# Optimization experiments

Hardware: AMD Instinct MI355X
Metric: run time of the kernel (lower is better)

Reference implementation:

```python
import jax, jax.numpy as jnp
import numpy as np


def setup_inputs() -> dict:
    key = jax.random.key(0)
    ks = jax.random.split(key, 4)
    B, C, H, W = 8, 256, 64, 64
    Cq = C // 8
    x = jax.random.normal(ks[0], (B, C, H, W), dtype=jnp.float32)
    wq = jax.random.normal(ks[1], (Cq, C), dtype=jnp.float32) * (1.0 / np.sqrt(C))
    bq = jnp.zeros((Cq,), dtype=jnp.float32)
    wk = jax.random.normal(ks[2], (Cq, C), dtype=jnp.float32) * (1.0 / np.sqrt(C))
    bk = jnp.zeros((Cq,), dtype=jnp.float32)
    wv = jax.random.normal(ks[3], (C, C), dtype=jnp.float32) * (1.0 / np.sqrt(C))
    bv = jnp.zeros((C,), dtype=jnp.float32)
    return {"x": x, "wq": wq, "bq": bq, "wk": wk, "bk": bk, "wv": wv, "bv": bv}


def reference(x, wq, bq, wk, bk, wv, bv):
    B, C, H, W = x.shape
    N = H * W
    xf = x.reshape(B, C, N)  # [B, C, N] ; 1x1 conv == channel matmul
    q = jnp.einsum('bcn,dc->bnd', xf, wq) + bq          # [B, N, Cq]
    k = jnp.einsum('bcn,dc->bdn', xf, wk) + bk[:, None]  # [B, Cq, N]
    v = jnp.einsum('bcn,dc->bdn', xf, wv) + bv[:, None]  # [B, C, N]
    energy = jnp.einsum('bnd,bdm->bnm', q, k)           # [B, N, N]
    attn = jax.nn.softmax(energy, axis=-1)              # softmax over keys
    # out[b,c,i] = sum_j v[b,c,j] * attn[b,i,j]
    out = jnp.einsum('bcj,bij->bci', v, attn).reshape(B, C, H, W)
    return x + out
```

## Files before the change

kernel.cpp:

```cpp
#include <hip/hip_runtime.h>


#define CH  256
#define DQ  32
#define NSP 4096
#define RWS 320

typedef short short8 __attribute__((ext_vector_type(8)));
typedef float float4v __attribute__((ext_vector_type(4)));

__device__ __forceinline__ unsigned short f2b(float f) {
  unsigned int u = __float_as_uint(f);
  unsigned int r = u + 0x7fffu + ((u >> 16) & 1u);
  return (unsigned short)(r >> 16);
}
__device__ __forceinline__ short8 ld8(const unsigned short* p) {
  return *(const short8*)p;
}

__global__ __launch_bounds__(256) void prep_kernel(
    const float* __restrict__ wq, const float* __restrict__ bq,
    const float* __restrict__ wk, const float* __restrict__ bk,
    const float* __restrict__ wv, const float* __restrict__ bv,
    unsigned short* __restrict__ wh, unsigned short* __restrict__ wl,
    float* __restrict__ ball) {
  int r = blockIdx.x, c = threadIdx.x;
  float v;
  if (r < 32)       v = wq[r * CH + c];
  else if (r < 64)  v = wk[(r - 32) * CH + c];
  else              v = wv[(r - 64) * CH + c];
  unsigned int u = __float_as_uint(v);
  unsigned short hi = (unsigned short)(u >> 16);
  float hf = __uint_as_float(u & 0xffff0000u);
  unsigned short lo = (unsigned short)(__float_as_uint(v - hf) >> 16);
  wh[r * CH + c] = hi;
  wl[r * CH + c] = lo;
  if (c == 0)
    ball[r] = (r < 32) ? bq[r] : (r < 64 ? bk[r - 32] : bv[r - 64]);
}

__device__ __forceinline__ void stage_x32(const float* xkn, float* buf,
                                          int w, int lane) {
  const int c = 8 * w + (lane >> 3);
  const int n = (4 * (lane & 7)) ^ ((w & 3) << 3);
  const float* gp = xkn + (size_t)c * NSP + n;
  __builtin_amdgcn_global_load_lds(
      (const __attribute__((address_space(1))) unsigned int*)gp,
      (__attribute__((address_space(3))) unsigned int*)(buf + w * 256),
      16, 0, 0);
}

__global__ __launch_bounds__(256, 3) void proj_kernel(
    const float* __restrict__ x,
    const unsigned short* __restrict__ wh, const unsigned short* __restrict__ wl,
    const float* __restrict__ ball,
    unsigned short* __restrict__ qb, unsigned short* __restrict__ kb,
    unsigned short* __restrict__ vb, int b0) {
  __shared__ float xs[2][1024];

  const int bz   = blockIdx.z;
  const int bg   = b0 + bz;
  const int n0   = blockIdx.x * 32;
  const int t    = threadIdx.x;
  const int w    = t >> 6;
  const int lane = t & 63;
  const int col  = lane & 15;
  const int quad = lane >> 4;
  const int r0   = 80 * w;
  const int rb0  = quad * 256 + (col ^ (8 * (quad & 1)));
  const int nsx  = quad >> 1;

  const float* xb = x + (size_t)bg * CH * NSP;

  float4v acc[5][2];
#pragma unroll
  for (int rf = 0; rf < 5; ++rf) {
    float bias = ball[r0 + 16 * rf + col];
#pragma unroll
    for (int ns = 0; ns < 2; ++ns)
      acc[rf][ns] = (float4v){bias, bias, bias, bias};
  }

  stage_x32(xb + n0, xs[0], w, lane);
  __syncthreads();
  int cur = 0;

#pragma unroll 1
  for (int ks = 0; ks < 8; ++ks) {
    const int k0 = ks * 32;
    if (ks < 7)
      stage_x32(xb + (size_t)(k0 + 32) * NSP + n0, xs[cur ^ 1], w, lane);

    short8 wfh[5], wfl[5];
#pragma unroll
    for (int rf = 0; rf < 5; ++rf) {
      size_t wo = (size_t)(r0 + 16 * rf + col) * CH + k0 + quad * 8;
      wfh[rf] = ld8(wh + wo);
      wfl[rf] = ld8(wl + wo);
    }

    const float* xc = &xs[cur][0];
    short8 ah[2], al[2];
#pragma unroll
    for (int nsb = 0; nsb < 2; ++nsb) {
      const float* xp2 = xc + rb0 + 16 * (nsb ^ nsx);
#pragma unroll
      for (int j = 0; j < 8; ++j) {
        float v = xp2[j * 32];
        unsigned int u = __float_as_uint(v);
        ah[nsb][j] = (short)(u >> 16);
        float hf = __uint_as_float(u & 0xffff0000u);
        al[nsb][j] = (short)(__float_as_uint(v - hf) >> 16);
      }
    }

#pragma unroll
    for (int rf = 0; rf < 5; ++rf)
#pragma unroll
      for (int ns = 0; ns < 2; ++ns) {
        acc[rf][ns] = __builtin_amdgcn_mfma_f32_16x16x32_bf16(ah[ns], wfh[rf], acc[rf][ns], 0, 0, 0);
        acc[rf][ns] = __builtin_amdgcn_mfma_f32_16x16x32_bf16(al[ns], wfh[rf], acc[rf][ns], 0, 0, 0);
        acc[rf][ns] = __builtin_amdgcn_mfma_f32_16x16x32_bf16(ah[ns], wfl[rf], acc[rf][ns], 0, 0, 0);
      }

    __syncthreads();
    cur ^= 1;
  }

#pragma unroll
  for (int rf = 0; rf < 5; ++rf) {
    const int rr = r0 + 16 * rf + col;
    const int rb = r0 + 16 * rf;
#pragma unroll
    for (int ns = 0; ns < 2; ++ns) {
      const int nb = n0 + ns * 16 + quad * 4;
      if (rb < 32) {
#pragma unroll
        for (int reg = 0; reg < 4; ++reg)
          qb[((size_t)bz * NSP + nb + reg) * DQ + rr] = f2b(acc[rf][ns][reg]);
      } else if (rb < 64) {
#pragma unroll
        for (int reg = 0; reg < 4; ++reg)
          kb[((size_t)bz * NSP + nb + reg) * DQ + (rr - 32)] = f2b(acc[rf][ns][reg]);
      } else {
        ushort4 o = {f2b(acc[rf][ns][0]), f2b(acc[rf][ns][1]),
                     f2b(acc[rf][ns][2]), f2b(acc[rf][ns][3])};
        *(ushort4*)&vb[((size_t)bz * CH + (rr - 64)) * NSP + nb] = o;
      }
    }
  }
}

__global__ __launch_bounds__(512, 4) void attn_kernel(
    const float* __restrict__ x,
    const unsigned short* __restrict__ qb, const unsigned short* __restrict__ kb,
    const unsigned short* __restrict__ vb,
    float* __restrict__ out, int b0, int ns) {
  __shared__ unsigned short ps[2 * 64 * 64];
  __shared__ float buf[4][64];
  __shared__ float lf[64];

  const int bl   = blockIdx.x % ns;
  const int bg   = b0 + bl;
  const int i0   = (blockIdx.x / ns) * 64;
  const int t    = threadIdx.x;
  const int w    = t >> 6;
  const int rh   = w >> 2;
  const int kq   = w & 3;
  const int lane = t & 63;
  const int col  = lane & 15;
  const int quad = lane >> 4;
  const float LOG2E = 1.4426950408889634f;
  const float MOFF  = 57.70780163555852f;

  const unsigned short* qbb = qb + (size_t)bl * NSP * DQ;
  const unsigned short* kbb = kb + (size_t)bl * NSP * DQ;
  const unsigned short* vbb = vb + (size_t)bl * CH * NSP;

  short8 qf[2];
#pragma unroll
  for (int rgp = 0; rgp < 2; ++rgp)
    qf[rgp] = ld8(qbb + (size_t)(i0 + 32 * rh + 16 * rgp + col) * DQ + quad * 8);
  const float4v z4 = (float4v){0.f, 0.f, 0.f, 0.f};

  const int kb8 = 2 * kq + (col >> 3);
  const int ci  = col & 7;
  const int q4  = 4 * (quad & 1);
  const int ob  = quad ^ ci;

  float4v acc[4][2];
#pragma unroll
  for (int rg = 0; rg < 4; ++rg)
#pragma unroll
    for (int ct = 0; ct < 2; ++ct) acc[rg][ct] = z4;
  float lp[2][4];
#pragma unroll
  for (int rgp = 0; rgp < 2; ++rgp)
#pragma unroll
    for (int reg = 0; reg < 4; ++reg) lp[rgp][reg] = 0.0f;

  short8 kf = ld8(kbb + (size_t)(16 * kq + col) * DQ + quad * 8);
  for (int j0 = 0; j0 < NSP; j0 += 64) {
    const int cp = (j0 >> 6) & 1;
    short8 vf[2][2];
#pragma unroll
    for (int ct = 0; ct < 2; ++ct)
#pragma unroll
      for (int h = 0; h < 2; ++h)
        vf[ct][h] = ld8(vbb + (size_t)(32 * w + 16 * ct + col) * NSP
                        + j0 + 32 * h + quad * 8);
    float4v c0 = __builtin_amdgcn_mfma_f32_16x16x32_bf16(qf[0], kf, z4, 0, 0, 0);
    float4v c1 = __builtin_amdgcn_mfma_f32_16x16x32_bf16(qf[1], kf, z4, 0, 0, 0);
    int jn = (j0 + 64 < NSP) ? j0 + 64 : 0;
    short8 kfn = ld8(kbb + (size_t)(jn + 16 * kq + col) * DQ + quad * 8);
    unsigned short* pw = &ps[cp * 4096 + (32 * rh + quad * 4) * 64 + ci];
#pragma unroll
    for (int reg = 0; reg < 4; ++reg) {
      float p0 = __builtin_amdgcn_exp2f(fmaf(c0[reg], LOG2E, -MOFF));
      float p1 = __builtin_amdgcn_exp2f(fmaf(c1[reg], LOG2E, -MOFF));
      lp[0][reg] += p0;
      lp[1][reg] += p1;
      const int so = reg * 64 + (kb8 ^ (q4 + reg)) * 8;
      pw[so]        = f2b(p0);
      pw[so + 1024] = f2b(p1);
    }
    __syncthreads();

    const short8* pb0 = (const short8*)&ps[cp * 4096 + col * 64 + ob * 8];
    const short8* pb1 = (const short8*)&ps[cp * 4096 + col * 64 + (ob ^ 4) * 8];
    __builtin_amdgcn_s_setprio(1);
#pragma unroll
    for (int rg = 0; rg < 4; ++rg) {
      short8 pf0 = pb0[rg * 128];
      short8 pf1 = pb1[rg * 128];
#pragma unroll
      for (int ct = 0; ct < 2; ++ct) {
        acc[rg][ct] = __builtin_amdgcn_mfma_f32_16x16x32_bf16(pf0, vf[ct][0], acc[rg][ct], 0, 0, 0);
        acc[rg][ct] = __builtin_amdgcn_mfma_f32_16x16x32_bf16(pf1, vf[ct][1], acc[rg][ct], 0, 0, 0);
      }
    }
    __builtin_amdgcn_s_setprio(0);
    kf = kfn;
  }

#pragma unroll
  for (int rgp = 0; rgp < 2; ++rgp)
#pragma unroll
    for (int reg = 0; reg < 4; ++reg) {
#pragma unroll
      for (int mask = 1; mask <= 8; mask <<= 1)
        lp[rgp][reg] += __shfl_xor(lp[rgp][reg], mask);
    }
  if (col == 0) {
#pragma unroll
    for (int rgp = 0; rgp < 2; ++rgp)
#pragma unroll
      for (int reg = 0; reg < 4; ++reg)
        buf[kq][32 * rh + 16 * rgp + quad * 4 + reg] = lp[rgp][reg];
  }
  __syncthreads();
  if (kq == 0 && col == 0) {
#pragma unroll
    for (int rgp = 0; rgp < 2; ++rgp)
#pragma unroll
      for (int reg = 0; reg < 4; ++reg) {
        int row = 32 * rh + 16 * rgp + quad * 4 + reg;
        lf[row] = 1.0f / (buf[0][row] + buf[1][row] + buf[2][row] + buf[3][row]);
      }
  }
  __syncthreads();

#pragma unroll
  for (int rg = 0; rg < 4; ++rg) {
    float linv[4];
#pragma unroll
    for (int reg = 0; reg < 4; ++reg)
      linv[reg] = lf[16 * rg + quad * 4 + reg];
#pragma unroll
    for (int ct = 0; ct < 2; ++ct) {
      int c  = 32 * w + 16 * ct + col;
      int ib = i0 + 16 * rg + quad * 4;
      size_t idx = ((size_t)bg * CH + c) * NSP + ib;
      float4 xr = *(const float4*)&x[idx];
      float4 o;
      o.x = acc[rg][ct][0] * linv[0] + xr.x;
      o.y = acc[rg][ct][1] * linv[1] + xr.y;
      o.z = acc[rg][ct][2] * linv[2] + xr.z;
      o.w = acc[rg][ct][3] * linv[3] + xr.w;
      *(float4*)&out[idx] = o;
    }
  }
}

extern "C" void kernel_launch(void* const* d_in, const int* in_sizes, int n_in,
                              void* d_out, int out_size, void* d_ws, size_t ws_size,
                              hipStream_t stream) {
  (void)in_sizes; (void)n_in; (void)out_size;
  const float* x  = (const float*)d_in[0];
  const float* wq = (const float*)d_in[1];
  const float* bq = (const float*)d_in[2];
  const float* wk = (const float*)d_in[3];
  const float* bk = (const float*)d_in[4];
  const float* wv = (const float*)d_in[5];
  const float* bv = (const float*)d_in[6];
  float* out = (float*)d_out;

  const size_t WALL_B = (size_t)RWS * CH * sizeof(float) + 4096;
  const size_t QB_B = (size_t)NSP * DQ * sizeof(unsigned short);
  const size_t VB_B = (size_t)CH * NSP * sizeof(unsigned short);
  const size_t PER_B = 2 * QB_B + VB_B;

  int ns = 8;
  while (ns > 1 && WALL_B + (size_t)ns * PER_B > ws_size) ns >>= 1;

  char* ws = (char*)d_ws;
  unsigned short* wh = (unsigned short*)ws;
  unsigned short* wl = wh + (size_t)RWS * CH;
  float* ball = (float*)(ws + (size_t)RWS * CH * 2 * sizeof(unsigned short));
  char* qkv = ws + WALL_B;
  unsigned short* qb = (unsigned short*)qkv;
  unsigned short* kb = (unsigned short*)(qkv + (size_t)ns * QB_B);
  unsigned short* vb = (unsigned short*)(qkv + (size_t)ns * 2 * QB_B);

  prep_kernel<<<dim3(RWS), dim3(256), 0, stream>>>(wq, bq, wk, bk, wv, bv, wh, wl, ball);
  for (int b0 = 0; b0 < 8; b0 += ns) {
    proj_kernel<<<dim3(128, 1, ns), dim3(256), 0, stream>>>(
        x, wh, wl, ball, qb, kb, vb, b0);
    attn_kernel<<<dim3(64 * ns), dim3(512), 0, stream>>>(
        x, qb, kb, vb, out, b0, ns);
  }
}
```

Baseline: 269.6 us.

## Widen projection tile with full-K LDS staging; shrink attention block to 32 rows

The projection kernel now processes 64 spatial positions per block and stages all eight 32-channel slices of x into LDS up front (64 KB), removing the per-step double-buffer syncs and doubling reuse of weight fragments. The attention kernel moves from 512-thread blocks covering 64 query rows to 256-thread blocks covering 32 rows, each wave owning 64 output channels and all 64 keys per tile, giving twice as many blocks. The trade-offs are lower proj occupancy from the large LDS footprint, more V loads per query row, and recomputation of QK energies across more blocks.

```diff
diff --git a/kernel.cpp b/kernel.cpp
--- a/kernel.cpp
+++ b/kernel.cpp
@@ -39,57 +39,62 @@
     ball[r] = (r < 32) ? bq[r] : (r < 64 ? bk[r - 32] : bv[r - 64]);
 }
 
-__device__ __forceinline__ void stage_x32(const float* xkn, float* buf,
-                                          int w, int lane) {
-  const int c = 8 * w + (lane >> 3);
-  const int n = (4 * (lane & 7)) ^ ((w & 3) << 3);
-  const float* gp = xkn + (size_t)c * NSP + n;
-  __builtin_amdgcn_global_load_lds(
-      (const __attribute__((address_space(1))) unsigned int*)gp,
-      (__attribute__((address_space(3))) unsigned int*)(buf + w * 256),
-      16, 0, 0);
-}
-
-__global__ __launch_bounds__(256, 3) void proj_kernel(
+__device__ __forceinline__ void stage_x(const float* xkn, float* buf,
+                                        int w, int lane) {
+#pragma unroll
+  for (int i = 0; i < 2; ++i) {
+    const int h  = 2 * w + i;
+    const int sw = ((h >> 1) & 1) * 16;
+    const int c  = h * 4 + (lane >> 4);
+    const int n  = ((lane & 15) * 4) ^ sw;
+    const float* gp = xkn + (size_t)c * NSP + n;
+    __builtin_amdgcn_global_load_lds(
+        (const __attribute__((address_space(1))) unsigned int*)gp,
+        (__attribute__((address_space(3))) unsigned int*)(buf + h * 256),
+        16, 0, 0);
+  }
+}
+
+__global__ __launch_bounds__(256, 2) void proj_kernel(
     const float* __restrict__ x,
     const unsigned short* __restrict__ wh, const unsigned short* __restrict__ wl,
     const float* __restrict__ ball,
     unsigned short* __restrict__ qb, unsigned short* __restrict__ kb,
     unsigned short* __restrict__ vb, int b0) {
-  __shared__ float xs[2][1024];
+  __shared__ float xs[8][2048];
 
   const int bz   = blockIdx.z;
   const int bg   = b0 + bz;
-  const int n0   = blockIdx.x * 32;
+  const int n0   = blockIdx.x * 64;
   const int t    = threadIdx.x;
   const int w    = t >> 6;
   const int lane = t & 63;
   const int col  = lane & 15;
   const int quad = lane >> 4;
   const int r0   = 80 * w;
-  const int rb0  = quad * 256 + (col ^ (8 * (quad & 1)));
-  const int nsx  = quad >> 1;
+  const int e    = (quad & 1) * 16;
+  const int lbase = quad * 512 + col;
 
   const float* xb = x + (size_t)bg * CH * NSP;
 
-  float4v acc[5][2];
+#pragma unroll
+  for (int ks = 0; ks < 8; ++ks)
+    stage_x(xb + (size_t)(ks * 32) * NSP + n0, xs[ks], w, lane);
+
+  float4v acc[5][4];
 #pragma unroll
   for (int rf = 0; rf < 5; ++rf) {
     float bias = ball[r0 + 16 * rf + col];
 #pragma unroll
-    for (int ns = 0; ns < 2; ++ns)
+    for (int ns = 0; ns < 4; ++ns)
       acc[rf][ns] = (float4v){bias, bias, bias, bias};
   }
 
-  stage_x32(xb + n0, xs[0], w, lane);
   __syncthreads();
-  int cur = 0;
-
-#pragma unroll 1
+
+#pragma unroll
   for (int ks = 0; ks < 8; ++ks) {
     const int k0 = ks * 32;
-    if (ks < 7)
-      stage_x32(xb + (size_t)(k0 + 32) * NSP + n0, xs[cur ^ 1], w, lane);
 
     short8 wfh[5], wfl[5];
 #pragma unroll
@@ -99,14 +104,14 @@
       wfl[rf] = ld8(wl + wo);
     }
 
-    const float* xc = &xs[cur][0];
-    short8 ah[2], al[2];
-#pragma unroll
-    for (int nsb = 0; nsb < 2; ++nsb) {
-      const float* xp2 = xc + rb0 + 16 * (nsb ^ nsx);
+    const float* xc = &xs[ks][0];
+    short8 ah[4], al[4];
+#pragma unroll
+    for (int nsb = 0; nsb < 4; ++nsb) {
+      const float* xp2 = xc + lbase + ((nsb * 16) ^ e);
 #pragma unroll
       for (int j = 0; j < 8; ++j) {
-        float v = xp2[j * 32];
+        float v = xp2[j * 64];
         unsigned int u = __float_as_uint(v);
         ah[nsb][j] = (short)(u >> 16);
         float hf = __uint_as_float(u & 0xffff0000u);
@@ -117,14 +122,11 @@
 #pragma unroll
     for (int rf = 0; rf < 5; ++rf)
 #pragma unroll
-      for (int ns = 0; ns < 2; ++ns) {
+      for (int ns = 0; ns < 4; ++ns) {
         acc[rf][ns] = __builtin_amdgcn_mfma_f32_16x16x32_bf16(ah[ns], wfh[rf], acc[rf][ns], 0, 0, 0);
         acc[rf][ns] = __builtin_amdgcn_mfma_f32_16x16x32_bf16(al[ns], wfh[rf], acc[rf][ns], 0, 0, 0);
         acc[rf][ns] = __builtin_amdgcn_mfma_f32_16x16x32_bf16(ah[ns], wfl[rf], acc[rf][ns], 0, 0, 0);
       }
-
-    __syncthreads();
-    cur ^= 1;
   }
 
 #pragma unroll
@@ -132,7 +134,7 @@
     const int rr = r0 + 16 * rf + col;
     const int rb = r0 + 16 * rf;
 #pragma unroll
-    for (int ns = 0; ns < 2; ++ns) {
+    for (int ns = 0; ns < 4; ++ns) {
       const int nb = n0 + ns * 16 + quad * 4;
       if (rb < 32) {
 #pragma unroll
@@ -151,22 +153,20 @@
   }
 }
 
-__global__ __launch_bounds__(512, 4) void attn_kernel(
+__global__ __launch_bounds__(256, 4) void attn_kernel(
     const float* __restrict__ x,
     const unsigned short* __restrict__ qb, const unsigned short* __restrict__ kb,
     const unsigned short* __restrict__ vb,
     float* __restrict__ out, int b0, int ns) {
-  __shared__ unsigned short ps[2 * 64 * 64];
-  __shared__ float buf[4][64];
-  __shared__ float lf[64];
+  __shared__ unsigned short ps[2 * 32 * 64];
+  __shared__ float buf[4][32];
+  __shared__ float lf[32];
 
   const int bl   = blockIdx.x % ns;
   const int bg   = b0 + bl;
-  const int i0   = (blockIdx.x / ns) * 64;
+  const int i0   = (blockIdx.x / ns) * 32;
   const int t    = threadIdx.x;
   const int w    = t >> 6;
-  const int rh   = w >> 2;
-  const int kq   = w & 3;
   const int lane = t & 63;
   const int col  = lane & 15;
   const int quad = lane >> 4;
@@ -180,40 +180,40 @@
   short8 qf[2];
 #pragma unroll
   for (int rgp = 0; rgp < 2; ++rgp)
-    qf[rgp] = ld8(qbb + (size_t)(i0 + 32 * rh + 16 * rgp + col) * DQ + quad * 8);
+    qf[rgp] = ld8(qbb + (size_t)(i0 + 16 * rgp + col) * DQ + quad * 8);
   const float4v z4 = (float4v){0.f, 0.f, 0.f, 0.f};
 
-  const int kb8 = 2 * kq + (col >> 3);
+  const int kb8 = 2 * w + (col >> 3);
   const int ci  = col & 7;
   const int q4  = 4 * (quad & 1);
   const int ob  = quad ^ ci;
 
-  float4v acc[4][2];
-#pragma unroll
-  for (int rg = 0; rg < 4; ++rg)
-#pragma unroll
-    for (int ct = 0; ct < 2; ++ct) acc[rg][ct] = z4;
+  float4v acc[2][4];
+#pragma unroll
+  for (int rg = 0; rg < 2; ++rg)
+#pragma unroll
+    for (int ct = 0; ct < 4; ++ct) acc[rg][ct] = z4;
   float lp[2][4];
 #pragma unroll
   for (int rgp = 0; rgp < 2; ++rgp)
 #pragma unroll
     for (int reg = 0; reg < 4; ++reg) lp[rgp][reg] = 0.0f;
 
-  short8 kf = ld8(kbb + (size_t)(16 * kq + col) * DQ + quad * 8);
+  short8 kf = ld8(kbb + (size_t)(16 * w + col) * DQ + quad * 8);
   for (int j0 = 0; j0 < NSP; j0 += 64) {
     const int cp = (j0 >> 6) & 1;
-    short8 vf[2][2];
-#pragma unroll
-    for (int ct = 0; ct < 2; ++ct)
+    short8 vf[4][2];
+#pragma unroll
+    for (int ct = 0; ct < 4; ++ct)
 #pragma unroll
       for (int h = 0; h < 2; ++h)
-        vf[ct][h] = ld8(vbb + (size_t)(32 * w + 16 * ct + col) * NSP
+        vf[ct][h] = ld8(vbb + (size_t)(64 * w + 16 * ct + col) * NSP
                         + j0 + 32 * h + quad * 8);
     float4v c0 = __builtin_amdgcn_mfma_f32_16x16x32_bf16(qf[0], kf, z4, 0, 0, 0);
     float4v c1 = __builtin_amdgcn_mfma_f32_16x16x32_bf16(qf[1], kf, z4, 0, 0, 0);
     int jn = (j0 + 64 < NSP) ? j0 + 64 : 0;
-    short8 kfn = ld8(kbb + (size_t)(jn + 16 * kq + col) * DQ + quad * 8);
-    unsigned short* pw = &ps[cp * 4096 + (32 * rh + quad * 4) * 64 + ci];
+    short8 kfn = ld8(kbb + (size_t)(jn + 16 * w + col) * DQ + quad * 8);
+    unsigned short* pw = &ps[cp * 2048 + (quad * 4) * 64 + ci];
 #pragma unroll
     for (int reg = 0; reg < 4; ++reg) {
       float p0 = __builtin_amdgcn_exp2f(fmaf(c0[reg], LOG2E, -MOFF));
@@ -226,15 +226,15 @@
     }
     __syncthreads();
 
-    const short8* pb0 = (const short8*)&ps[cp * 4096 + col * 64 + ob * 8];
-    const short8* pb1 = (const short8*)&ps[cp * 4096 + col * 64 + (ob ^ 4) * 8];
+    const short8* pb0 = (const short8*)&ps[cp * 2048 + col * 64 + ob * 8];
+    const short8* pb1 = (const short8*)&ps[cp * 2048 + col * 64 + (ob ^ 4) * 8];
     __builtin_amdgcn_s_setprio(1);
 #pragma unroll
-    for (int rg = 0; rg < 4; ++rg) {
+    for (int rg = 0; rg < 2; ++rg) {
       short8 pf0 = pb0[rg * 128];
       short8 pf1 = pb1[rg * 128];
 #pragma unroll
-      for (int ct = 0; ct < 2; ++ct) {
+      for (int ct = 0; ct < 4; ++ct) {
         acc[rg][ct] = __builtin_amdgcn_mfma_f32_16x16x32_bf16(pf0, vf[ct][0], acc[rg][ct], 0, 0, 0);
         acc[rg][ct] = __builtin_amdgcn_mfma_f32_16x16x32_bf16(pf1, vf[ct][1], acc[rg][ct], 0, 0, 0);
       }
@@ -256,29 +256,29 @@
     for (int rgp = 0; rgp < 2; ++rgp)
 #pragma unroll
       for (int reg = 0; reg < 4; ++reg)
-        buf[kq][32 * rh + 16 * rgp + quad * 4 + reg] = lp[rgp][reg];
+        buf[w][16 * rgp + quad * 4 + reg] = lp[rgp][reg];
   }
   __syncthreads();
-  if (kq == 0 && col == 0) {
+  if (w == 0 && col == 0) {
 #pragma unroll
     for (int rgp = 0; rgp < 2; ++rgp)
 #pragma unroll
       for (int reg = 0; reg < 4; ++reg) {
-        int row = 32 * rh + 16 * rgp + quad * 4 + reg;
+        int row = 16 * rgp + quad * 4 + reg;
         lf[row] = 1.0f / (buf[0][row] + buf[1][row] + buf[2][row] + buf[3][row]);
       }
   }
   __syncthreads();
 
 #pragma unroll
-  for (int rg = 0; rg < 4; ++rg) {
+  for (int rg = 0; rg < 2; ++rg) {
     float linv[4];
 #pragma unroll
     for (int reg = 0; reg < 4; ++reg)
       linv[reg] = lf[16 * rg + quad * 4 + reg];
 #pragma unroll
-    for (int ct = 0; ct < 2; ++ct) {
-      int c  = 32 * w + 16 * ct + col;
+    for (int ct = 0; ct < 4; ++ct) {
+      int c  = 64 * w + 16 * ct + col;
       int ib = i0 + 16 * rg + quad * 4;
       size_t idx = ((size_t)bg * CH + c) * NSP + ib;
       float4 xr = *(const float4*)&x[idx];
@@ -324,9 +324,9 @@
 
   prep_kernel<<<dim3(RWS), dim3(256), 0, stream>>>(wq, bq, wk, bk, wv, bv, wh, wl, ball);
   for (int b0 = 0; b0 < 8; b0 += ns) {
-    proj_kernel<<<dim3(128, 1, ns), dim3(256), 0, stream>>>(
+    proj_kernel<<<dim3(64, 1, ns), dim3(256), 0, stream>>>(
         x, wh, wl, ball, qb, kb, vb, b0);
-    attn_kernel<<<dim3(64 * ns), dim3(512), 0, stream>>>(
+    attn_kernel<<<dim3(128 * ns), dim3(256), 0, stream>>>(
         x, qb, kb, vb, out, b0, ns);
   }
 }
```

Measured after the change: 361.5 us. 34.1% more time.

## Stage full x tile up front and transpose Q/K stores through LDS

Applied to the files above, without the earlier changes.

The projection kernel now issues all eight x K-slices into a 32KB LDS buffer at once, replacing the double-buffered loop, so the loop has a single barrier rather than one per step. Weight fragments are loaded in groups of two to cut register pressure, and the occupancy hint rises from 3 to 4 blocks. Q/K results are transposed through LDS so they can be written as vectorized ushort4 rows instead of scattered 2-byte stores. The cost is more LDS per block, which may limit occupancy, and the XOR bank swizzle on x staging is removed, which may bring back LDS bank conflicts.

```diff
diff --git a/kernel.cpp b/kernel.cpp
--- a/kernel.cpp
+++ b/kernel.cpp
@@ -42,7 +42,7 @@
 __device__ __forceinline__ void stage_x32(const float* xkn, float* buf,
                                           int w, int lane) {
   const int c = 8 * w + (lane >> 3);
-  const int n = (4 * (lane & 7)) ^ ((w & 3) << 3);
+  const int n = (lane & 7) * 4;
   const float* gp = xkn + (size_t)c * NSP + n;
   __builtin_amdgcn_global_load_lds(
       (const __attribute__((address_space(1))) unsigned int*)gp,
@@ -50,13 +50,13 @@
       16, 0, 0);
 }
 
-__global__ __launch_bounds__(256, 3) void proj_kernel(
+__global__ __launch_bounds__(256, 4) void proj_kernel(
     const float* __restrict__ x,
     const unsigned short* __restrict__ wh, const unsigned short* __restrict__ wl,
     const float* __restrict__ ball,
     unsigned short* __restrict__ qb, unsigned short* __restrict__ kb,
     unsigned short* __restrict__ vb, int b0) {
-  __shared__ float xs[2][1024];
+  __shared__ float xs[8][1024];
 
   const int bz   = blockIdx.z;
   const int bg   = b0 + bz;
@@ -67,86 +67,106 @@
   const int col  = lane & 15;
   const int quad = lane >> 4;
   const int r0   = 80 * w;
-  const int rb0  = quad * 256 + (col ^ (8 * (quad & 1)));
-  const int nsx  = quad >> 1;
 
   const float* xb = x + (size_t)bg * CH * NSP;
+
+#pragma unroll
+  for (int ks = 0; ks < 8; ++ks)
+    stage_x32(xb + (size_t)(ks * 32) * NSP + n0, xs[ks], w, lane);
 
   float4v acc[5][2];
 #pragma unroll
   for (int rf = 0; rf < 5; ++rf) {
     float bias = ball[r0 + 16 * rf + col];
 #pragma unroll
-    for (int ns = 0; ns < 2; ++ns)
-      acc[rf][ns] = (float4v){bias, bias, bias, bias};
-  }
-
-  stage_x32(xb + n0, xs[0], w, lane);
+    for (int g = 0; g < 2; ++g)
+      acc[rf][g] = (float4v){bias, bias, bias, bias};
+  }
+
   __syncthreads();
-  int cur = 0;
 
 #pragma unroll 1
   for (int ks = 0; ks < 8; ++ks) {
     const int k0 = ks * 32;
-    if (ks < 7)
-      stage_x32(xb + (size_t)(k0 + 32) * NSP + n0, xs[cur ^ 1], w, lane);
-
-    short8 wfh[5], wfl[5];
-#pragma unroll
-    for (int rf = 0; rf < 5; ++rf) {
-      size_t wo = (size_t)(r0 + 16 * rf + col) * CH + k0 + quad * 8;
-      wfh[rf] = ld8(wh + wo);
-      wfl[rf] = ld8(wl + wo);
-    }
-
-    const float* xc = &xs[cur][0];
+
+    const float* xc = &xs[ks][0];
     short8 ah[2], al[2];
 #pragma unroll
-    for (int nsb = 0; nsb < 2; ++nsb) {
-      const float* xp2 = xc + rb0 + 16 * (nsb ^ nsx);
+    for (int g = 0; g < 2; ++g)
 #pragma unroll
       for (int j = 0; j < 8; ++j) {
-        float v = xp2[j * 32];
+        float v = xc[(quad * 8 + j) * 32 + 16 * g + col];
         unsigned int u = __float_as_uint(v);
-        ah[nsb][j] = (short)(u >> 16);
+        ah[g][j] = (short)(u >> 16);
         float hf = __uint_as_float(u & 0xffff0000u);
-        al[nsb][j] = (short)(__float_as_uint(v - hf) >> 16);
-      }
-    }
-
-#pragma unroll
-    for (int rf = 0; rf < 5; ++rf)
-#pragma unroll
-      for (int ns = 0; ns < 2; ++ns) {
-        acc[rf][ns] = __builtin_amdgcn_mfma_f32_16x16x32_bf16(ah[ns], wfh[rf], acc[rf][ns], 0, 0, 0);
-        acc[rf][ns] = __builtin_amdgcn_mfma_f32_16x16x32_bf16(al[ns], wfh[rf], acc[rf][ns], 0, 0, 0);
-        acc[rf][ns] = __builtin_amdgcn_mfma_f32_16x16x32_bf16(ah[ns], wfl[rf], acc[rf][ns], 0, 0, 0);
-      }
-
-    __syncthreads();
-    cur ^= 1;
-  }
+        al[g][j] = (short)(__float_as_uint(v - hf) >> 16);
+      }
+
+#pragma unroll
+    for (int grp = 0; grp < 3; ++grp) {
+      const int rfb = grp * 2;
+      const int nrf = (grp == 2) ? 1 : 2;
+      short8 wfh[2], wfl[2];
+#pragma unroll
+      for (int i = 0; i < 2; ++i) {
+        if (i < nrf) {
+          size_t wo = (size_t)(r0 + 16 * (rfb + i) + col) * CH + k0 + quad * 8;
+          wfh[i] = ld8(wh + wo);
+          wfl[i] = ld8(wl + wo);
+        }
+      }
+#pragma unroll
+      for (int i = 0; i < 2; ++i) {
+        if (i < nrf) {
+#pragma unroll
+          for (int g = 0; g < 2; ++g) {
+            acc[rfb + i][g] = __builtin_amdgcn_mfma_f32_16x16x32_bf16(ah[g], wfh[i], acc[rfb + i][g], 0, 0, 0);
+            acc[rfb + i][g] = __builtin_amdgcn_mfma_f32_16x16x32_bf16(al[g], wfh[i], acc[rfb + i][g], 0, 0, 0);
+            acc[rfb + i][g] = __builtin_amdgcn_mfma_f32_16x16x32_bf16(ah[g], wfl[i], acc[rfb + i][g], 0, 0, 0);
+          }
+        }
+      }
+    }
+  }
+
+  __syncthreads();
 
 #pragma unroll
   for (int rf = 0; rf < 5; ++rf) {
     const int rr = r0 + 16 * rf + col;
     const int rb = r0 + 16 * rf;
-#pragma unroll
-    for (int ns = 0; ns < 2; ++ns) {
-      const int nb = n0 + ns * 16 + quad * 4;
-      if (rb < 32) {
+    if (rb >= 64) {
+#pragma unroll
+      for (int g = 0; g < 2; ++g) {
+        const int nb = n0 + 16 * g + quad * 4;
+        ushort4 o = {f2b(acc[rf][g][0]), f2b(acc[rf][g][1]),
+                     f2b(acc[rf][g][2]), f2b(acc[rf][g][3])};
+        *(ushort4*)&vb[((size_t)bz * CH + (rr - 64)) * NSP + nb] = o;
+      }
+    }
+  }
+
+  if (w == 0) {
+    unsigned short* qt = (unsigned short*)&xs[0][0];
+#pragma unroll
+    for (int rf = 0; rf < 4; ++rf) {
+      const int rr = 16 * rf + col;
+#pragma unroll
+      for (int g = 0; g < 2; ++g) {
 #pragma unroll
         for (int reg = 0; reg < 4; ++reg)
-          qb[((size_t)bz * NSP + nb + reg) * DQ + rr] = f2b(acc[rf][ns][reg]);
-      } else if (rb < 64) {
-#pragma unroll
-        for (int reg = 0; reg < 4; ++reg)
-          kb[((size_t)bz * NSP + nb + reg) * DQ + (rr - 32)] = f2b(acc[rf][ns][reg]);
-      } else {
-        ushort4 o = {f2b(acc[rf][ns][0]), f2b(acc[rf][ns][1]),
-                     f2b(acc[rf][ns][2]), f2b(acc[rf][ns][3])};
-        *(ushort4*)&vb[((size_t)bz * CH + (rr - 64)) * NSP + nb] = o;
-      }
+          qt[(16 * g + quad * 4 + reg) * 68 + rr] = f2b(acc[rf][g][reg]);
+      }
+    }
+    const int c4 = (lane & 15) * 4;
+#pragma unroll
+    for (int it = 0; it < 8; ++it) {
+      const int n = 4 * it + quad;
+      ushort4 vv = *(const ushort4*)&qt[n * 68 + c4];
+      if (c4 < 32)
+        *(ushort4*)&qb[((size_t)bz * NSP + n0 + n) * DQ + c4] = vv;
+      else
+        *(ushort4*)&kb[((size_t)bz * NSP + n0 + n) * DQ + (c4 - 32)] = vv;
     }
   }
 }
```

New measurement: 269.6 us. No clear change (-0.0%).
